# Kernel tuning notes

Hardware: AMD Instinct MI355X
Metric: run time of the kernel (lower is better)

Reference implementation:

```python
import jax, jax.numpy as jnp
from jax import lax
import numpy as np

H, W = 64, 64
K = 5                 # LO_kernel_size
SIGMA = 0.5           # LO_sigma
CHAN_PER_POS = 8
INIT_STRIDE = 16
BATCH = 32


def _num_offsets(h, w, s):
    ny = (h - s) // s * 2 + 1
    nx = (w - s) // s * 2 + 1
    return ny, nx, ny * nx - 1  # use_origin=False drops (0,0)


def setup_inputs() -> dict:
    key = jax.random.key(0)
    k1, k2 = jax.random.split(key)
    ny, nx, npos = _num_offsets(H, W, INIT_STRIDE)
    C = npos * CHAN_PER_POS
    x = jax.random.normal(k1, (BATCH, C, H, W), dtype=jnp.float32)
    # init_offset(): grid of (iw*stride, ih*stride), skipping origin
    offs = []
    for ih in range(-(ny // 2), ny // 2 + 1):
        for iw in range(-(nx // 2), nx // 2 + 1):
            if ih == 0 and iw == 0:
                continue
            offs.append([iw * INIT_STRIDE, ih * INIT_STRIDE])
    offset = jnp.asarray(np.array(offs, dtype=np.float32))
    # perturb so suboffsets (fractional part) are nonzero, as after training
    offset = offset + jax.random.uniform(k2, offset.shape, dtype=jnp.float32,
                                         minval=-0.4, maxval=0.4)
    return {"x": x, "offset": offset}


def _displace(x, off_int):
    # x: (B, P, Cpp, H, W); off_int: (P, 2) int32 (dx, dy)
    # out[y, x] = in[y - dy, x - dx], zero outside (integer shift by +offset)
    _, _, _, h, w = x.shape

    def shift_one(xp, dxy):
        dx, dy = dxy[0], dxy[1]
        ys = jnp.arange(h) - dy
        xs = jnp.arange(w) - dx
        ym = (ys >= 0) & (ys < h)
        xm = (xs >= 0) & (xs < w)
        ysc = jnp.clip(ys, 0, h - 1)
        xsc = jnp.clip(xs, 0, w - 1)
        out = xp[:, :, ysc][:, :, :, xsc]
        return out * (ym[:, None] & xm[None, :]).astype(xp.dtype)

    return jax.vmap(shift_one, in_axes=(1, 0), out_axes=1)(x, off_int)


def reference(x, offset) -> jnp.ndarray:
    B, C, h, w = x.shape
    P = offset.shape[0]
    cpp = C // P  # bind_chan

    off_round = jnp.round(offset)
    off_int = off_round.astype(jnp.int32)

    # integer-part displacement per channel group
    disp = _displace(x.reshape(B, P, cpp, h, w), off_int).reshape(B, C, h, w)

    # fractional part -> gaussian interpolation kernel (offset.dim()==2 path)
    sub = offset - lax.stop_gradient(off_round)          # (P, 2) = (subx, suby)
    c = K // 2
    jj, ii = jnp.meshgrid(jnp.arange(K, dtype=jnp.float32) - c,
                          jnp.arange(K, dtype=jnp.float32) - c, indexing='xy')
    field = jnp.stack([jj, ii], axis=-1)                 # (K, K, 2): (x, y)
    d = field[None] + sub[:, None, None, :]              # (P, K, K, 2)
    kernel = jnp.exp(-jnp.sum(d * d, axis=-1) / (2.0 * SIGMA ** 2))
    kernel = kernel / jnp.sum(kernel, axis=(1, 2), keepdims=True)

    # depthwise conv: each per-position kernel shared by bind_chan channels
    kw = jnp.repeat(kernel, cpp, axis=0)[:, None]        # (C, 1, K, K)
    out = lax.conv_general_dilated(
        disp, kw, window_strides=(1, 1), padding=[(c, c), (c, c)],
        feature_group_count=C,
        dimension_numbers=('NCHW', 'OIHW', 'NCHW'))
    return out
```

## Files before the change

### kernel.cpp

```cpp
#include <hip/hip_runtime.h>
#include <math.h>

#define HH 64
#define WW 64
#define KS 5
#define CPP 8
#define NPOS 48
#define CHAN (NPOS * CPP)
#define NBATCH 32

__global__ __launch_bounds__(256)
void displace_sep_kernel(const float* __restrict__ x,
                         const float* __restrict__ off,
                         float* __restrict__ out)
{
    const int bp = blockIdx.x;
    const int p  = bp % NPOS;
    const int b  = bp / NPOS;

    const int t  = threadIdx.x;
    const int tx = t & 7;
    const int ty = (t >> 3) & 3;
    const int cc = t >> 5;

    const int x0 = tx * 8;
    const int y0 = ty * 16;

    const size_t plane = ((size_t)b * CHAN + (size_t)p * CPP + (size_t)cc) * (HH * WW);
    const float* __restrict__ src = x + plane;
    float* __restrict__ dst = out + plane;

    const float offx = off[2 * p + 0];
    const float offy = off[2 * p + 1];
    const float rx = rintf(offx), ry = rintf(offy);
    const int   dx = (int)rx,     dy = (int)ry;
    const float subx = offx - rx, suby = offy - ry;

    float wx[KS], wy[KS];
    float sumx = 0.f, sumy = 0.f;
    #pragma unroll
    for (int k = 0; k < KS; ++k) {
        const float ax = (float)(k - 2) + subx;
        const float ay = (float)(k - 2) + suby;
        wx[k] = __expf(-2.0f * ax * ax);
        wy[k] = __expf(-2.0f * ay * ay);
        sumx += wx[k];
        sumy += wy[k];
    }
    const float inv = 1.0f / (sumx * sumy);
    #pragma unroll
    for (int k = 0; k < KS; ++k) wx[k] *= inv;

    int   saddr[12];
    float smask[12];
    #pragma unroll
    for (int j = 0; j < 12; ++j) {
        const int xx = x0 - 2 + j;
        const int sx = xx - dx;
        const bool ok = ((unsigned)xx < (unsigned)WW) && ((unsigned)sx < (unsigned)WW);
        saddr[j] = ok ? sx : 0;
        smask[j] = ok ? 1.0f : 0.0f;
    }

    float hb[5][8];

    #pragma unroll
    for (int i = 0; i < 20; ++i) {
        const int yy = y0 - 2 + i;
        const int sy = yy - dy;
        const bool rowok = ((unsigned)yy < (unsigned)HH) && ((unsigned)sy < (unsigned)HH);
        float (&h)[8] = hb[i % 5];
        if (rowok) {
            const float* __restrict__ row = src + sy * WW;
            float s[12];
            #pragma unroll
            for (int j = 0; j < 12; ++j)
                s[j] = row[saddr[j]] * smask[j];
            #pragma unroll
            for (int j = 0; j < 8; ++j) {
                float a = wx[0] * s[j];
                a = fmaf(wx[1], s[j + 1], a);
                a = fmaf(wx[2], s[j + 2], a);
                a = fmaf(wx[3], s[j + 3], a);
                a = fmaf(wx[4], s[j + 4], a);
                h[j] = a;
            }
        } else {
            #pragma unroll
            for (int j = 0; j < 8; ++j) h[j] = 0.0f;
        }

        if (i >= 4) {
            const int y = y0 + i - 4;
            float acc[8];
            #pragma unroll
            for (int j = 0; j < 8; ++j) acc[j] = 0.0f;
            #pragma unroll
            for (int ky = 0; ky < KS; ++ky) {
                const float w = wy[ky];
                float (&hr)[8] = hb[(i - 4 + ky) % 5];
                #pragma unroll
                for (int j = 0; j < 8; ++j)
                    acc[j] = fmaf(w, hr[j], acc[j]);
            }
            float4* o4 = (float4*)(dst + (size_t)y * WW + x0);
            o4[0] = make_float4(acc[0], acc[1], acc[2], acc[3]);
            o4[1] = make_float4(acc[4], acc[5], acc[6], acc[7]);
        }
    }
}

extern "C" void kernel_launch(void* const* d_in, const int* in_sizes, int n_in,
                              void* d_out, int out_size, void* d_ws, size_t ws_size,
                              hipStream_t stream) {
    const float* x   = (const float*)d_in[0];
    const float* off = (const float*)d_in[1];
    float* out = (float*)d_out;

    const int blocks = NBATCH * NPOS;
    displace_sep_kernel<<<blocks, 256, 0, stream>>>(x, off, out);
}
```

Before: 381.5 us.

## Map one wavefront per half-plane row strip with lane shuffles for horizontal taps

Work is reassigned so each 64-lane wavefront handles half of one channel plane, with each lane owning one column. Horizontal neighbours come from cross-lane shuffles instead of each thread loading a 12-wide halo, which gives fully coalesced row loads and stores. The intent is to remove redundant halo loads and uncoalesced scalar accesses in this memory-bound depthwise blur. In exchange it adds four shuffles per row, and each 32-row strip reloads 4 halo rows.

```diff
diff --git a/kernel.cpp b/kernel.cpp
--- a/kernel.cpp
+++ b/kernel.cpp
@@ -8,104 +8,83 @@
 #define NPOS 48
 #define CHAN (NPOS * CPP)
 #define NBATCH 32
+#define STRIP 32
 
 __global__ __launch_bounds__(256)
-void displace_sep_kernel(const float* __restrict__ x,
-                         const float* __restrict__ off,
-                         float* __restrict__ out)
+void displace_wave_kernel(const float* __restrict__ x,
+                          const float* __restrict__ off,
+                          float* __restrict__ out)
 {
-    const int bp = blockIdx.x;
-    const int p  = bp % NPOS;
-    const int b  = bp / NPOS;
+    const int t    = threadIdx.x;
+    const int lane = t & 63;
+    const int gw   = blockIdx.x * 4 + (t >> 6);
+    const int half = gw & 1;
+    const int plane = gw >> 1;
+    const int p    = (plane % CHAN) / CPP;
 
-    const int t  = threadIdx.x;
-    const int tx = t & 7;
-    const int ty = (t >> 3) & 3;
-    const int cc = t >> 5;
-
-    const int x0 = tx * 8;
-    const int y0 = ty * 16;
-
-    const size_t plane = ((size_t)b * CHAN + (size_t)p * CPP + (size_t)cc) * (HH * WW);
-    const float* __restrict__ src = x + plane;
-    float* __restrict__ dst = out + plane;
+    const float* __restrict__ src = x   + (size_t)plane * (HH * WW);
+    float*       __restrict__ dst = out + (size_t)plane * (HH * WW);
 
     const float offx = off[2 * p + 0];
     const float offy = off[2 * p + 1];
-    const float rx = rintf(offx), ry = rintf(offy);
-    const int   dx = (int)rx,     dy = (int)ry;
-    const float subx = offx - rx, suby = offy - ry;
+    const float rxf = rintf(offx), ryf = rintf(offy);
+    const int   dx = (int)rxf,     dy = (int)ryf;
+    const float subx = offx - rxf, suby = offy - ryf;
 
-    float wx[KS], wy[KS];
+    float wxr[KS], wy[KS];
     float sumx = 0.f, sumy = 0.f;
     #pragma unroll
     for (int k = 0; k < KS; ++k) {
         const float ax = (float)(k - 2) + subx;
         const float ay = (float)(k - 2) + suby;
-        wx[k] = __expf(-2.0f * ax * ax);
-        wy[k] = __expf(-2.0f * ay * ay);
-        sumx += wx[k];
+        wxr[k] = __expf(-2.0f * ax * ax);
+        wy[k]  = __expf(-2.0f * ay * ay);
+        sumx += wxr[k];
         sumy += wy[k];
     }
     const float inv = 1.0f / (sumx * sumy);
+
+    float wxm[KS];
     #pragma unroll
-    for (int k = 0; k < KS; ++k) wx[k] *= inv;
-
-    int   saddr[12];
-    float smask[12];
-    #pragma unroll
-    for (int j = 0; j < 12; ++j) {
-        const int xx = x0 - 2 + j;
-        const int sx = xx - dx;
-        const bool ok = ((unsigned)xx < (unsigned)WW) && ((unsigned)sx < (unsigned)WW);
-        saddr[j] = ok ? sx : 0;
-        smask[j] = ok ? 1.0f : 0.0f;
+    for (int k = 0; k < KS; ++k) {
+        const int sl = lane + (k - 2);
+        wxm[k] = ((unsigned)sl < (unsigned)WW) ? wxr[k] * inv : 0.0f;
     }
 
-    float hb[5][8];
+    const int   sx  = lane - dx;
+    const float mx  = ((unsigned)sx < (unsigned)WW) ? 1.0f : 0.0f;
+    const int   sxc = min(max(sx, 0), WW - 1);
+
+    const int y0 = half * STRIP;
+    float hb[5];
 
     #pragma unroll
-    for (int i = 0; i < 20; ++i) {
+    for (int i = 0; i < STRIP + 4; ++i) {
         const int yy = y0 - 2 + i;
         const int sy = yy - dy;
-        const bool rowok = ((unsigned)yy < (unsigned)HH) && ((unsigned)sy < (unsigned)HH);
-        float (&h)[8] = hb[i % 5];
-        if (rowok) {
-            const float* __restrict__ row = src + sy * WW;
-            float s[12];
-            #pragma unroll
-            for (int j = 0; j < 12; ++j)
-                s[j] = row[saddr[j]] * smask[j];
-            #pragma unroll
-            for (int j = 0; j < 8; ++j) {
-                float a = wx[0] * s[j];
-                a = fmaf(wx[1], s[j + 1], a);
-                a = fmaf(wx[2], s[j + 2], a);
-                a = fmaf(wx[3], s[j + 3], a);
-                a = fmaf(wx[4], s[j + 4], a);
-                h[j] = a;
-            }
-        } else {
-            #pragma unroll
-            for (int j = 0; j < 8; ++j) h[j] = 0.0f;
+        float h = 0.0f;
+        if (((unsigned)yy < (unsigned)HH) & ((unsigned)sy < (unsigned)HH)) {
+            const float v   = src[sy * WW + sxc] * mx;
+            const float sm2 = __shfl(v, (lane + 62) & 63);
+            const float sm1 = __shfl(v, (lane + 63) & 63);
+            const float sp1 = __shfl(v, (lane + 1)  & 63);
+            const float sp2 = __shfl(v, (lane + 2)  & 63);
+            h = wxm[0] * sm2;
+            h = fmaf(wxm[1], sm1, h);
+            h = fmaf(wxm[2], v,   h);
+            h = fmaf(wxm[3], sp1, h);
+            h = fmaf(wxm[4], sp2, h);
         }
+        hb[i % 5] = h;
 
         if (i >= 4) {
             const int y = y0 + i - 4;
-            float acc[8];
-            #pragma unroll
-            for (int j = 0; j < 8; ++j) acc[j] = 0.0f;
-            #pragma unroll
-            for (int ky = 0; ky < KS; ++ky) {
-                const float w = wy[ky];
-                float (&hr)[8] = hb[(i - 4 + ky) % 5];
-                #pragma unroll
-                for (int j = 0; j < 8; ++j)
-                    acc[j] = fmaf(w, hr[j], acc[j]);
-            }
-            float4* o4 = (float4*)(dst + (size_t)y * WW + x0);
-            o4[0] = make_float4(acc[0], acc[1], acc[2], acc[3]);
-            o4[1] = make_float4(acc[4], acc[5], acc[6], acc[7]);
+            float a = wy[0] * hb[(i - 4) % 5];
+            a = fmaf(wy[1], hb[(i - 3) % 5], a);
+            a = fmaf(wy[2], hb[(i - 2) % 5], a);
+            a = fmaf(wy[3], hb[(i - 1) % 5], a);
+            a = fmaf(wy[4], hb[(i - 0) % 5], a);
+            dst[y * WW + lane] = a;
         }
     }
 }
@@ -117,6 +96,6 @@
     const float* off = (const float*)d_in[1];
     float* out = (float*)d_out;
 
-    const int blocks = NBATCH * NPOS;
-    displace_sep_kernel<<<blocks, 256, 0, stream>>>(x, off, out);
+    const int blocks = NBATCH * CHAN * 2 / 4;
+    displace_wave_kernel<<<blocks, 256, 0, stream>>>(x, off, out);
 }
```

After: 349.8 us. 8.3% less time.
